# Kernel optimization log

Measured on AMD Instinct MI355X. Metric: run time of the kernel, lower is better.

The kernel has to match this reference:

```python
import jax, jax.numpy as jnp
import numpy as np

D = 2048      # hidden_size
H = 1408      # moe_intermediate_size
E = 8         # n_routed_experts
B, S = 2, 2048


def setup_inputs() -> dict:
    key = jax.random.key(0)
    ks = jax.random.split(key, 5)
    scale = 1.0 / np.sqrt(D)
    return {
        "hidden_states": jax.random.normal(ks[0], (B, S, D), dtype=jnp.float32),
        "Wg": jax.random.normal(ks[1], (E, D), dtype=jnp.float32) * scale,   # gate proj
        "W1": jax.random.normal(ks[2], (E, H, D), dtype=jnp.float32) * scale,  # expert gate_proj
        "W3": jax.random.normal(ks[3], (E, H, D), dtype=jnp.float32) * scale,  # expert up_proj
        "W2": jax.random.normal(ks[4], (E, D, H), dtype=jnp.float32) * (1.0 / np.sqrt(H)),  # expert down_proj
        "top_k": 2,
    }


def reference(hidden_states, Wg, W1, W3, W2, top_k):
    b, s, d = hidden_states.shape
    x = hidden_states.reshape(-1, d)                      # [T, D]
    # --- gate: softmax over expert logits, top-k selection ---
    scores = jax.nn.softmax(x @ Wg.T, axis=-1)            # [T, E]
    topk_w, topk_idx = jax.lax.top_k(scores, top_k)       # [T, K]
    # per-token combine weights over experts; zero for unselected experts
    combine = jnp.sum(jax.nn.one_hot(topk_idx, E, dtype=x.dtype) * topk_w[..., None], axis=1)  # [T, E]
    # --- experts: SwiGLU MLP, masked/weighted combine ---
    y = jnp.zeros_like(x)
    for i in range(E):
        h = jax.nn.silu(x @ W1[i].T) * (x @ W3[i].T)      # [T, H]
        y = y + combine[:, i:i + 1] * (h @ W2[i].T)       # [T, D]
    return y.reshape(b, s, d) + hidden_states
```

## Files before the change

### kernel.cpp

```cpp
#include <hip/hip_runtime.h>
#include <stdint.h>

#define DD 2048
#define HH 1408
#define EE 8
#define TT 4096

#define BM 128
#define BN 64
#define BK 64
#define MAXBLK 72
#define NB1 22
#define NB2 32
#define NW8 2883584

using floatx4 = __attribute__((ext_vector_type(4))) float;
using bf16x8  = __attribute__((ext_vector_type(8))) __bf16;

__device__ __forceinline__ unsigned int pack_bf16(float a, float b) {
    unsigned int ua = __float_as_uint(a) + 0x8000u;
    unsigned int ub = __float_as_uint(b) + 0x8000u;
    return __builtin_amdgcn_perm(ub, ua, 0x07060302u);
}
__device__ __forceinline__ unsigned short f2bf(float a) {
    return (unsigned short)((__float_as_uint(a) + 0x8000u) >> 16);
}

__device__ __forceinline__ void gld16(const unsigned short* g, unsigned short* l) {
    __builtin_amdgcn_global_load_lds(
        (__attribute__((address_space(1))) void*)g,
        (__attribute__((address_space(3))) void*)l, 16, 0, 0);
}

__device__ __forceinline__ int xcd_swz(int bid, int live) {
    int xcd = bid & 7, pos = bid >> 3;
    int q = live >> 3, r = live & 7;
    return (xcd < r ? xcd * (q + 1) : r * (q + 1) + (xcd - r) * q) + pos;
}

__global__ __launch_bounds__(256) void k_prep(const float* __restrict__ W1,
                                              const float* __restrict__ W3,
                                              const float* __restrict__ W2,
                                              unsigned short* __restrict__ W1b,
                                              unsigned short* __restrict__ W3b,
                                              unsigned short* __restrict__ W2b,
                                              int* __restrict__ counts,
                                              int* __restrict__ cursor) {
    if (blockIdx.x == 0 && threadIdx.x < 16) {
        if (threadIdx.x < 8) counts[threadIdx.x] = 0;
        else                 cursor[threadIdx.x - 8] = 0;
    }
    int i = blockIdx.x * 256 + threadIdx.x;
    if (i >= 3 * NW8) return;
    const float* s; unsigned short* d; int off;
    if (i < NW8)          { s = W1; d = W1b; off = i; }
    else if (i < 2 * NW8) { s = W3; d = W3b; off = i - NW8; }
    else                  { s = W2; d = W2b; off = i - 2 * NW8; }
    const float4* s4 = (const float4*)s + (size_t)off * 2;
    float4 a = s4[0], b = s4[1];
    uint4 o;
    o.x = pack_bf16(a.x, a.y); o.y = pack_bf16(a.z, a.w);
    o.z = pack_bf16(b.x, b.y); o.w = pack_bf16(b.z, b.w);
    *(uint4*)(d + (size_t)off * 8) = o;
}

__global__ __launch_bounds__(256) void k_gate(const float* __restrict__ x,
                                              const float* __restrict__ Wg,
                                              unsigned short* __restrict__ Xb,
                                              float* __restrict__ out,
                                              int* __restrict__ topk_i,
                                              float* __restrict__ topk_w,
                                              int* __restrict__ counts) {
    const int t = blockIdx.x;
    const int tid = threadIdx.x;
    const float4* xr = (const float4*)(x + (size_t)t * DD);
    float4* orow = (float4*)(out + (size_t)t * DD);
    uint2* xbrow = (uint2*)(Xb + (size_t)t * DD);
    const float4* wg4 = (const float4*)Wg;
    float p[EE];
#pragma unroll
    for (int e = 0; e < EE; ++e) p[e] = 0.f;
#pragma unroll
    for (int it = 0; it < (DD / 4) / 256; ++it) {
        int d4 = it * 256 + tid;
        float4 xv = xr[d4];
        orow[d4] = xv;
        uint2 pk;
        pk.x = pack_bf16(xv.x, xv.y);
        pk.y = pack_bf16(xv.z, xv.w);
        xbrow[d4] = pk;
#pragma unroll
        for (int e = 0; e < EE; ++e) {
            float4 wv = wg4[e * (DD / 4) + d4];
            p[e] += xv.x * wv.x + xv.y * wv.y + xv.z * wv.z + xv.w * wv.w;
        }
    }
#pragma unroll
    for (int e = 0; e < EE; ++e) {
#pragma unroll
        for (int off = 32; off; off >>= 1) p[e] += __shfl_xor(p[e], off);
    }
    __shared__ float red[4][EE];
    const int wave = tid >> 6, lane = tid & 63;
    if (lane == 0) {
#pragma unroll
        for (int e = 0; e < EE; ++e) red[wave][e] = p[e];
    }
    __syncthreads();
    if (tid == 0) {
        float lg[EE];
#pragma unroll
        for (int e = 0; e < EE; ++e) lg[e] = red[0][e] + red[1][e] + red[2][e] + red[3][e];
        float mx = lg[0];
#pragma unroll
        for (int e = 1; e < EE; ++e) mx = fmaxf(mx, lg[e]);
        float den = 0.f, pr[EE];
#pragma unroll
        for (int e = 0; e < EE; ++e) { pr[e] = __expf(lg[e] - mx); den += pr[e]; }
        float inv = 1.f / den;
#pragma unroll
        for (int e = 0; e < EE; ++e) pr[e] *= inv;
        int i0 = 0; float v0 = pr[0];
#pragma unroll
        for (int e = 1; e < EE; ++e) if (pr[e] > v0) { v0 = pr[e]; i0 = e; }
        int i1 = -1; float v1 = -1.f;
#pragma unroll
        for (int e = 0; e < EE; ++e) if (e != i0 && pr[e] > v1) { v1 = pr[e]; i1 = e; }
        topk_i[t * 2 + 0] = i0; topk_i[t * 2 + 1] = i1;
        topk_w[t * 2 + 0] = v0; topk_w[t * 2 + 1] = v1;
        atomicAdd(&counts[i0], 1);
        atomicAdd(&counts[i1], 1);
    }
}

__global__ void k_scan(const int* __restrict__ counts, int* __restrict__ offs,
                       int* __restrict__ blk_e, int* __restrict__ blk_m,
                       int* __restrict__ nblk) {
    if (threadIdx.x == 0) {
        int s = 0, nb = 0;
        for (int e = 0; e < EE; ++e) {
            offs[e] = s;
            int c = counts[e];
            for (int m = 0; m < c; m += BM) { blk_e[nb] = e; blk_m[nb] = m; ++nb; }
            s += c;
        }
        *nblk = nb;
        for (int i = nb; i < MAXBLK; ++i) { blk_e[i] = 0; blk_m[i] = 0; }
    }
}

__global__ __launch_bounds__(256) void k_compact(const int* __restrict__ topk_i,
                                                 const float* __restrict__ topk_w,
                                                 const int* __restrict__ offs,
                                                 int* __restrict__ cursor,
                                                 int* __restrict__ tok_id,
                                                 float* __restrict__ tok_w) {
    const int t = blockIdx.x * 256 + threadIdx.x;
    if (t >= TT) return;
#pragma unroll
    for (int k = 0; k < 2; ++k) {
        int e = topk_i[t * 2 + k];
        int slot = atomicAdd(&cursor[e], 1);
        int p = offs[e] + slot;
        tok_id[p] = t;
        tok_w[p] = topk_w[t * 2 + k];
    }
}

__global__ __launch_bounds__(256, 2) void k_gemm1(const unsigned short* __restrict__ Xb,
                                                  const unsigned short* __restrict__ W1b,
                                                  const unsigned short* __restrict__ W3b,
                                                  const int* __restrict__ counts,
                                                  const int* __restrict__ offs,
                                                  const int* __restrict__ blk_e,
                                                  const int* __restrict__ blk_m,
                                                  const int* __restrict__ nblk,
                                                  const int* __restrict__ tok_id,
                                                  unsigned short* __restrict__ hbuf) {
    const int live = *nblk * NB1;
    int bid = blockIdx.x;
    if (bid >= live) return;
    bid = xcd_swz(bid, live);
    const int b   = bid / NB1;
    const int e   = blk_e[b];
    const int m0  = blk_m[b];
    const int cnt = counts[e];
    const int n0  = (bid % NB1) * BN;
    const int seg = offs[e];
    const int tid = threadIdx.x;

    __shared__ __align__(16) unsigned short Xs[2][BM * 64];
    __shared__ __align__(16) unsigned short W1s[2][BN * 64];
    __shared__ __align__(16) unsigned short W3s[2][BN * 64];
    __shared__ int ids[BM];

    if (tid < BM) ids[tid] = tok_id[seg + min(m0 + tid, cnt - 1)];
    __syncthreads();

    const int lane = tid & 63, wave = tid >> 6;
    const int lr = lane >> 3, lc = lane & 7;
    const int quad = lane >> 4, l16 = lane & 15;
    const int wm = wave >> 1, wn = wave & 1;

    const unsigned short* xp[4];
#pragma unroll
    for (int j = 0; j < 4; ++j) {
        int rl = wave * 32 + j * 8 + lr;
        xp[j] = Xb + (size_t)ids[rl] * DD + (lc ^ (rl & 7)) * 8;
    }
    const unsigned short* w1p[2];
    const unsigned short* w3p[2];
#pragma unroll
    for (int j = 0; j < 2; ++j) {
        int rl = wave * 16 + j * 8 + lr;
        size_t ro = ((size_t)e * HH + n0 + rl) * DD + (lc ^ (rl & 7)) * 8;
        w1p[j] = W1b + ro;
        w3p[j] = W3b + ro;
    }

    floatx4 acc1[4][2], acc3[4][2];
#pragma unroll
    for (int i = 0; i < 4; ++i)
#pragma unroll
        for (int j = 0; j < 2; ++j) { acc1[i][j] = (floatx4)(0.f); acc3[i][j] = (floatx4)(0.f); }

    auto stage = [&](int buf, int k0) {
#pragma unroll
        for (int j = 0; j < 4; ++j)
            gld16(xp[j] + k0, &Xs[buf][(wave * 32 + j * 8) * 64]);
#pragma unroll
        for (int j = 0; j < 2; ++j) {
            gld16(w1p[j] + k0, &W1s[buf][(wave * 16 + j * 8) * 64]);
            gld16(w3p[j] + k0, &W3s[buf][(wave * 16 + j * 8) * 64]);
        }
    };

    stage(0, 0);
    __syncthreads();
    int cur = 0;
    for (int k0 = 0; k0 < DD; k0 += BK) {
        if (k0 + BK < DD) stage(cur ^ 1, k0 + BK);
#pragma unroll
        for (int kk = 0; kk < 2; ++kk) {
            bf16x8 a[4], b1[2], b3[2];
#pragma unroll
            for (int mf = 0; mf < 4; ++mf) {
                int r = wm * 64 + mf * 16 + l16;
                int s = (quad + kk * 4) ^ (r & 7);
                a[mf] = *(const bf16x8*)&Xs[cur][r * 64 + s * 8];
            }
#pragma unroll
            for (int nf = 0; nf < 2; ++nf) {
                int r = wn * 32 + nf * 16 + l16;
                int s = (quad + kk * 4) ^ (r & 7);
                b1[nf] = *(const bf16x8*)&W1s[cur][r * 64 + s * 8];
                b3[nf] = *(const bf16x8*)&W3s[cur][r * 64 + s * 8];
            }
#pragma unroll
            for (int mf = 0; mf < 4; ++mf)
#pragma unroll
                for (int nf = 0; nf < 2; ++nf) {
                    acc1[mf][nf] = __builtin_amdgcn_mfma_f32_16x16x32_bf16(a[mf], b1[nf], acc1[mf][nf], 0, 0, 0);
                    acc3[mf][nf] = __builtin_amdgcn_mfma_f32_16x16x32_bf16(a[mf], b3[nf], acc3[mf][nf], 0, 0, 0);
                }
        }
        __syncthreads();
        cur ^= 1;
    }
#pragma unroll
    for (int mf = 0; mf < 4; ++mf)
#pragma unroll
        for (int reg = 0; reg < 4; ++reg) {
            int m = wm * 64 + mf * 16 + quad * 4 + reg;
            if (m0 + m < cnt) {
                size_t row = (size_t)(seg + m0 + m) * HH + n0 + wn * 32;
#pragma unroll
                for (int nf = 0; nf < 2; ++nf) {
                    float c1 = acc1[mf][nf][reg];
                    float c3 = acc3[mf][nf][reg];
                    float hv = (c1 / (1.f + __expf(-c1))) * c3;
                    hbuf[row + nf * 16 + l16] = f2bf(hv);
                }
            }
        }
}

__global__ __launch_bounds__(256, 3) void k_gemm2(const unsigned short* __restrict__ hbuf,
                                                  const unsigned short* __restrict__ W2b,
                                                  const int* __restrict__ counts,
                                                  const int* __restrict__ offs,
                                                  const int* __restrict__ blk_e,
                                                  const int* __restrict__ blk_m,
                                                  const int* __restrict__ nblk,
                                                  const int* __restrict__ tok_id,
                                                  const float* __restrict__ tok_w,
                                                  float* __restrict__ out) {
    const int live = *nblk * NB2;
    int bid = blockIdx.x;
    if (bid >= live) return;
    bid = xcd_swz(bid, live);
    const int b   = bid / NB2;
    const int e   = blk_e[b];
    const int m0  = blk_m[b];
    const int cnt = counts[e];
    const int n0  = (bid % NB2) * BN;
    const int seg = offs[e];
    const int tid = threadIdx.x;

    __shared__ __align__(16) unsigned short As[2][BM * 64];
    __shared__ __align__(16) unsigned short Bs[2][BN * 64];
    __shared__ int ids[BM];
    __shared__ float wts[BM];

    if (tid < BM) {
        int rc = min(m0 + tid, cnt - 1);
        ids[tid] = tok_id[seg + rc];
        wts[tid] = tok_w[seg + rc];
    }
    __syncthreads();

    const int lane = tid & 63, wave = tid >> 6;
    const int lr = lane >> 3, lc = lane & 7;
    const int quad = lane >> 4, l16 = lane & 15;
    const int wm = wave >> 1, wn = wave & 1;

    const unsigned short* ap[4];
#pragma unroll
    for (int j = 0; j < 4; ++j) {
        int rl = wave * 32 + j * 8 + lr;
        ap[j] = hbuf + (size_t)(seg + min(m0 + rl, cnt - 1)) * HH + (lc ^ (rl & 7)) * 8;
    }
    const unsigned short* bp[2];
#pragma unroll
    for (int j = 0; j < 2; ++j) {
        int rl = wave * 16 + j * 8 + lr;
        bp[j] = W2b + ((size_t)e * DD + n0 + rl) * HH + (lc ^ (rl & 7)) * 8;
    }

    floatx4 acc[4][2];
#pragma unroll
    for (int i = 0; i < 4; ++i)
#pragma unroll
        for (int j = 0; j < 2; ++j) acc[i][j] = (floatx4)(0.f);

    auto stage = [&](int buf, int k0) {
#pragma unroll
        for (int j = 0; j < 4; ++j)
            gld16(ap[j] + k0, &As[buf][(wave * 32 + j * 8) * 64]);
#pragma unroll
        for (int j = 0; j < 2; ++j)
            gld16(bp[j] + k0, &Bs[buf][(wave * 16 + j * 8) * 64]);
    };

    stage(0, 0);
    __syncthreads();
    int cur = 0;
    for (int k0 = 0; k0 < HH; k0 += BK) {
        if (k0 + BK < HH) stage(cur ^ 1, k0 + BK);
#pragma unroll
        for (int kk = 0; kk < 2; ++kk) {
            bf16x8 a[4], bb[2];
#pragma unroll
            for (int mf = 0; mf < 4; ++mf) {
                int r = wm * 64 + mf * 16 + l16;
                int s = (quad + kk * 4) ^ (r & 7);
                a[mf] = *(const bf16x8*)&As[cur][r * 64 + s * 8];
            }
#pragma unroll
            for (int nf = 0; nf < 2; ++nf) {
                int r = wn * 32 + nf * 16 + l16;
                int s = (quad + kk * 4) ^ (r & 7);
                bb[nf] = *(const bf16x8*)&Bs[cur][r * 64 + s * 8];
            }
#pragma unroll
            for (int mf = 0; mf < 4; ++mf)
#pragma unroll
                for (int nf = 0; nf < 2; ++nf)
                    acc[mf][nf] = __builtin_amdgcn_mfma_f32_16x16x32_bf16(a[mf], bb[nf], acc[mf][nf], 0, 0, 0);
        }
        __syncthreads();
        cur ^= 1;
    }
#pragma unroll
    for (int mf = 0; mf < 4; ++mf)
#pragma unroll
        for (int reg = 0; reg < 4; ++reg) {
            int m = wm * 64 + mf * 16 + quad * 4 + reg;
            if (m0 + m < cnt) {
                int token = ids[m];
                float w = wts[m];
                float* orow = out + (size_t)token * DD + n0 + wn * 32;
#pragma unroll
                for (int nf = 0; nf < 2; ++nf)
                    atomicAdd(orow + nf * 16 + l16, w * acc[mf][nf][reg]);
            }
        }
}

extern "C" void kernel_launch(void* const* d_in, const int* in_sizes, int n_in,
                              void* d_out, int out_size, void* d_ws, size_t ws_size,
                              hipStream_t stream) {
    const float* x  = (const float*)d_in[0];
    const float* Wg = (const float*)d_in[1];
    const float* W1 = (const float*)d_in[2];
    const float* W3 = (const float*)d_in[3];
    const float* W2 = (const float*)d_in[4];
    float* out = (float*)d_out;

    int*   counts = (int*)d_ws;
    int*   cursor = counts + 8;
    int*   offs   = cursor + 8;
    int*   blk_e  = offs + 8;
    int*   blk_m  = blk_e + MAXBLK;
    int*   nblk   = blk_m + MAXBLK;
    int*   topk_i = nblk + 8;
    float* topk_w = (float*)(topk_i + 2 * TT);
    int*   tok_id = (int*)(topk_w + 2 * TT);
    float* tok_w  = (float*)(tok_id + 2 * TT);
    unsigned short* hbuf = (unsigned short*)(tok_w + 2 * TT);
    unsigned short* Xb   = hbuf + (size_t)2 * TT * HH;
    unsigned short* W1b  = Xb + (size_t)TT * DD;
    unsigned short* W3b  = W1b + (size_t)EE * HH * DD;
    unsigned short* W2b  = W3b + (size_t)EE * HH * DD;

    k_prep<<<(3 * NW8) / 256, 256, 0, stream>>>(W1, W3, W2, W1b, W3b, W2b, counts, cursor);
    k_gate<<<TT, 256, 0, stream>>>(x, Wg, Xb, out, topk_i, topk_w, counts);
    k_scan<<<1, 64, 0, stream>>>(counts, offs, blk_e, blk_m, nblk);
    k_compact<<<TT / 256, 256, 0, stream>>>(topk_i, topk_w, offs, cursor, tok_id, tok_w);
    k_gemm1<<<MAXBLK * NB1, 256, 0, stream>>>(Xb, W1b, W3b, counts, offs,
                                              blk_e, blk_m, nblk, tok_id, hbuf);
    k_gemm2<<<MAXBLK * NB2, 256, 0, stream>>>(hbuf, W2b, counts, offs,
                                              blk_e, blk_m, nblk, tok_id, tok_w, out);
}
```

Baseline: 710.6 us.

## Widen GEMM tiles to 128x128 and drop LDS double buffering

Both expert GEMMs now use a 128x128 output tile. In gemm1 the W1 and W3 rows are interleaved into a single B tile, and gemm2 covers 128 output columns per block, halving NB2. The LDS double buffer is removed in favour of a single buffer with a barrier after each load, and gemm1's occupancy hint rises to 3. The wider tiles give more MFMA work per LDS load and fewer blocks, but the single-buffered loop no longer overlaps global loads with compute, and register pressure grows with 16 accumulators.

```diff
diff --git a/kernel.cpp b/kernel.cpp
--- a/kernel.cpp
+++ b/kernel.cpp
@@ -7,11 +7,10 @@
 #define TT 4096
 
 #define BM 128
-#define BN 64
 #define BK 64
 #define MAXBLK 72
 #define NB1 22
-#define NB2 32
+#define NB2 16
 #define NW8 2883584
 
 using floatx4 = __attribute__((ext_vector_type(4))) float;
@@ -167,7 +166,7 @@
     }
 }
 
-__global__ __launch_bounds__(256, 2) void k_gemm1(const unsigned short* __restrict__ Xb,
+__global__ __launch_bounds__(256, 3) void k_gemm1(const unsigned short* __restrict__ Xb,
                                                   const unsigned short* __restrict__ W1b,
                                                   const unsigned short* __restrict__ W3b,
                                                   const int* __restrict__ counts,
@@ -185,13 +184,12 @@
     const int e   = blk_e[b];
     const int m0  = blk_m[b];
     const int cnt = counts[e];
-    const int n0  = (bid % NB1) * BN;
+    const int n0  = (bid % NB1) * 64;
     const int seg = offs[e];
     const int tid = threadIdx.x;
 
-    __shared__ __align__(16) unsigned short Xs[2][BM * 64];
-    __shared__ __align__(16) unsigned short W1s[2][BN * 64];
-    __shared__ __align__(16) unsigned short W3s[2][BN * 64];
+    __shared__ __align__(16) unsigned short Xs[BM * 64];
+    __shared__ __align__(16) unsigned short Bs[BM * 64];
     __shared__ int ids[BM];
 
     if (tid < BM) ids[tid] = tok_id[seg + min(m0 + tid, cnt - 1)];
@@ -206,66 +204,52 @@
 #pragma unroll
     for (int j = 0; j < 4; ++j) {
         int rl = wave * 32 + j * 8 + lr;
-        xp[j] = Xb + (size_t)ids[rl] * DD + (lc ^ (rl & 7)) * 8;
-    }
-    const unsigned short* w1p[2];
-    const unsigned short* w3p[2];
-#pragma unroll
-    for (int j = 0; j < 2; ++j) {
-        int rl = wave * 16 + j * 8 + lr;
-        size_t ro = ((size_t)e * HH + n0 + rl) * DD + (lc ^ (rl & 7)) * 8;
-        w1p[j] = W1b + ro;
-        w3p[j] = W3b + ro;
-    }
-
-    floatx4 acc1[4][2], acc3[4][2];
+        xp[j] = Xb + (size_t)ids[rl] * DD + (lc ^ lr) * 8;
+    }
+    const unsigned short* bpp[4];
+#pragma unroll
+    for (int j = 0; j < 4; ++j) {
+        const unsigned short* base = (j < 2) ? W1b : W3b;
+        int row = n0 + wave * 16 + (j & 1) * 8 + lr;
+        bpp[j] = base + ((size_t)e * HH + row) * DD + (lc ^ lr) * 8;
+    }
+
+    floatx4 acc[4][4];
 #pragma unroll
     for (int i = 0; i < 4; ++i)
 #pragma unroll
-        for (int j = 0; j < 2; ++j) { acc1[i][j] = (floatx4)(0.f); acc3[i][j] = (floatx4)(0.f); }
-
-    auto stage = [&](int buf, int k0) {
+        for (int j = 0; j < 4; ++j) acc[i][j] = (floatx4)(0.f);
+
+    for (int k0 = 0; k0 < DD; k0 += BK) {
 #pragma unroll
         for (int j = 0; j < 4; ++j)
-            gld16(xp[j] + k0, &Xs[buf][(wave * 32 + j * 8) * 64]);
-#pragma unroll
-        for (int j = 0; j < 2; ++j) {
-            gld16(w1p[j] + k0, &W1s[buf][(wave * 16 + j * 8) * 64]);
-            gld16(w3p[j] + k0, &W3s[buf][(wave * 16 + j * 8) * 64]);
-        }
-    };
-
-    stage(0, 0);
-    __syncthreads();
-    int cur = 0;
-    for (int k0 = 0; k0 < DD; k0 += BK) {
-        if (k0 + BK < DD) stage(cur ^ 1, k0 + BK);
+            gld16(xp[j] + k0, &Xs[(wave * 32 + j * 8) * 64]);
+#pragma unroll
+        for (int j = 0; j < 4; ++j)
+            gld16(bpp[j] + k0, &Bs[(wave * 32 + j * 8) * 64]);
+        __syncthreads();
 #pragma unroll
         for (int kk = 0; kk < 2; ++kk) {
-            bf16x8 a[4], b1[2], b3[2];
+            bf16x8 a[4], bb[4];
 #pragma unroll
             for (int mf = 0; mf < 4; ++mf) {
                 int r = wm * 64 + mf * 16 + l16;
                 int s = (quad + kk * 4) ^ (r & 7);
-                a[mf] = *(const bf16x8*)&Xs[cur][r * 64 + s * 8];
-            }
-#pragma unroll
-            for (int nf = 0; nf < 2; ++nf) {
-                int r = wn * 32 + nf * 16 + l16;
+                a[mf] = *(const bf16x8*)&Xs[r * 64 + s * 8];
+            }
+#pragma unroll
+            for (int nf = 0; nf < 4; ++nf) {
+                int r = wn * 64 + nf * 16 + l16;
                 int s = (quad + kk * 4) ^ (r & 7);
-                b1[nf] = *(const bf16x8*)&W1s[cur][r * 64 + s * 8];
-                b3[nf] = *(const bf16x8*)&W3s[cur][r * 64 + s * 8];
+                bb[nf] = *(const bf16x8*)&Bs[r * 64 + s * 8];
             }
 #pragma unroll
             for (int mf = 0; mf < 4; ++mf)
 #pragma unroll
-                for (int nf = 0; nf < 2; ++nf) {
-                    acc1[mf][nf] = __builtin_amdgcn_mfma_f32_16x16x32_bf16(a[mf], b1[nf], acc1[mf][nf], 0, 0, 0);
-                    acc3[mf][nf] = __builtin_amdgcn_mfma_f32_16x16x32_bf16(a[mf], b3[nf], acc3[mf][nf], 0, 0, 0);
-                }
+                for (int nf = 0; nf < 4; ++nf)
+                    acc[mf][nf] = __builtin_amdgcn_mfma_f32_16x16x32_bf16(a[mf], bb[nf], acc[mf][nf], 0, 0, 0);
         }
         __syncthreads();
-        cur ^= 1;
     }
 #pragma unroll
     for (int mf = 0; mf < 4; ++mf)
@@ -274,13 +258,12 @@
             int m = wm * 64 + mf * 16 + quad * 4 + reg;
             if (m0 + m < cnt) {
                 size_t row = (size_t)(seg + m0 + m) * HH + n0 + wn * 32;
-#pragma unroll
-                for (int nf = 0; nf < 2; ++nf) {
-                    float c1 = acc1[mf][nf][reg];
-                    float c3 = acc3[mf][nf][reg];
-                    float hv = (c1 / (1.f + __expf(-c1))) * c3;
-                    hbuf[row + nf * 16 + l16] = f2bf(hv);
-                }
+                float c1a = acc[mf][0][reg], c3a = acc[mf][1][reg];
+                float c1b = acc[mf][2][reg], c3b = acc[mf][3][reg];
+                float hva = (c1a / (1.f + __expf(-c1a))) * c3a;
+                float hvb = (c1b / (1.f + __expf(-c1b))) * c3b;
+                hbuf[row + l16]      = f2bf(hva);
+                hbuf[row + 16 + l16] = f2bf(hvb);
             }
         }
 }
@@ -303,12 +286,12 @@
     const int e   = blk_e[b];
     const int m0  = blk_m[b];
     const int cnt = counts[e];
-    const int n0  = (bid % NB2) * BN;
+    const int n0  = (bid % NB2) * 128;
     const int seg = offs[e];
     const int tid = threadIdx.x;
 
-    __shared__ __align__(16) unsigned short As[2][BM * 64];
-    __shared__ __align__(16) unsigned short Bs[2][BN * 64];
+    __shared__ __align__(16) unsigned short As[BM * 64];
+    __shared__ __align__(16) unsigned short Bs[BM * 64];
     __shared__ int ids[BM];
     __shared__ float wts[BM];
 
@@ -328,58 +311,51 @@
 #pragma unroll
     for (int j = 0; j < 4; ++j) {
         int rl = wave * 32 + j * 8 + lr;
-        ap[j] = hbuf + (size_t)(seg + min(m0 + rl, cnt - 1)) * HH + (lc ^ (rl & 7)) * 8;
-    }
-    const unsigned short* bp[2];
-#pragma unroll
-    for (int j = 0; j < 2; ++j) {
-        int rl = wave * 16 + j * 8 + lr;
-        bp[j] = W2b + ((size_t)e * DD + n0 + rl) * HH + (lc ^ (rl & 7)) * 8;
-    }
-
-    floatx4 acc[4][2];
+        ap[j] = hbuf + (size_t)(seg + min(m0 + rl, cnt - 1)) * HH + (lc ^ lr) * 8;
+    }
+    const unsigned short* bp[4];
+#pragma unroll
+    for (int j = 0; j < 4; ++j) {
+        int row = n0 + wave * 32 + j * 8 + lr;
+        bp[j] = W2b + ((size_t)e * DD + row) * HH + (lc ^ lr) * 8;
+    }
+
+    floatx4 acc[4][4];
 #pragma unroll
     for (int i = 0; i < 4; ++i)
 #pragma unroll
-        for (int j = 0; j < 2; ++j) acc[i][j] = (floatx4)(0.f);
-
-    auto stage = [&](int buf, int k0) {
+        for (int j = 0; j < 4; ++j) acc[i][j] = (floatx4)(0.f);
+
+    for (int k0 = 0; k0 < HH; k0 += BK) {
 #pragma unroll
         for (int j = 0; j < 4; ++j)
-            gld16(ap[j] + k0, &As[buf][(wave * 32 + j * 8) * 64]);
-#pragma unroll
-        for (int j = 0; j < 2; ++j)
-            gld16(bp[j] + k0, &Bs[buf][(wave * 16 + j * 8) * 64]);
-    };
-
-    stage(0, 0);
-    __syncthreads();
-    int cur = 0;
-    for (int k0 = 0; k0 < HH; k0 += BK) {
-        if (k0 + BK < HH) stage(cur ^ 1, k0 + BK);
+            gld16(ap[j] + k0, &As[(wave * 32 + j * 8) * 64]);
+#pragma unroll
+        for (int j = 0; j < 4; ++j)
+            gld16(bp[j] + k0, &Bs[(wave * 32 + j * 8) * 64]);
+        __syncthreads();
 #pragma unroll
         for (int kk = 0; kk < 2; ++kk) {
-            bf16x8 a[4], bb[2];
+            bf16x8 a[4], bb[4];
 #pragma unroll
             for (int mf = 0; mf < 4; ++mf) {
                 int r = wm * 64 + mf * 16 + l16;
                 int s = (quad + kk * 4) ^ (r & 7);
-                a[mf] = *(const bf16x8*)&As[cur][r * 64 + s * 8];
-            }
-#pragma unroll
-            for (int nf = 0; nf < 2; ++nf) {
-                int r = wn * 32 + nf * 16 + l16;
+                a[mf] = *(const bf16x8*)&As[r * 64 + s * 8];
+            }
+#pragma unroll
+            for (int nf = 0; nf < 4; ++nf) {
+                int r = wn * 64 + nf * 16 + l16;
                 int s = (quad + kk * 4) ^ (r & 7);
-                bb[nf] = *(const bf16x8*)&Bs[cur][r * 64 + s * 8];
+                bb[nf] = *(const bf16x8*)&Bs[r * 64 + s * 8];
             }
 #pragma unroll
             for (int mf = 0; mf < 4; ++mf)
 #pragma unroll
-                for (int nf = 0; nf < 2; ++nf)
+                for (int nf = 0; nf < 4; ++nf)
                     acc[mf][nf] = __builtin_amdgcn_mfma_f32_16x16x32_bf16(a[mf], bb[nf], acc[mf][nf], 0, 0, 0);
         }
         __syncthreads();
-        cur ^= 1;
     }
 #pragma unroll
     for (int mf = 0; mf < 4; ++mf)
@@ -389,9 +365,9 @@
             if (m0 + m < cnt) {
                 int token = ids[m];
                 float w = wts[m];
-                float* orow = out + (size_t)token * DD + n0 + wn * 32;
-#pragma unroll
-                for (int nf = 0; nf < 2; ++nf)
+                float* orow = out + (size_t)token * DD + n0 + wn * 64;
+#pragma unroll
+                for (int nf = 0; nf < 4; ++nf)
                     atomicAdd(orow + nf * 16 + l16, w * acc[mf][nf][reg]);
             }
         }
```

New measurement: 687.2 us. -3.3%, faster.
